# Kernel optimization log

Hardware: AMD Instinct MI355X
Metric: run time of the kernel (lower is better)

The kernel has to match this reference:

```python
import jax, jax.numpy as jnp
import numpy as np

B, S, D, F, E, K = 4, 2048, 512, 1024, 8, 2

def setup_inputs() -> dict:
    key = jax.random.key(0)
    ks = jax.random.split(key, 7)
    hidden = jax.random.normal(ks[0], (B, S, D), dtype=jnp.float32)
    top_k_indices = jax.random.randint(ks[1], (B, S, K), 0, E, dtype=jnp.int32)
    top_k_weights = jax.random.uniform(ks[2], (B, S, K), dtype=jnp.float32)
    scale1 = 1.0 / np.sqrt(D)
    scale2 = 1.0 / np.sqrt(F)
    W1 = jax.random.normal(ks[3], (E, D, F), dtype=jnp.float32) * scale1
    b1 = jnp.zeros((E, F), dtype=jnp.float32)
    W2 = jax.random.normal(ks[4], (E, F, D), dtype=jnp.float32) * scale2
    b2 = jnp.zeros((E, D), dtype=jnp.float32)
    return {"hidden": hidden, "top_k_indices": top_k_indices,
            "top_k_weights": top_k_weights, "W1": W1, "b1": b1, "W2": W2, "b2": b2}

def reference(hidden, top_k_indices, top_k_weights, W1, b1, W2, b2):
    b, s, d = hidden.shape
    e = W1.shape[0]
    x = hidden.reshape(-1, d)                      # [T, D]
    idx = top_k_indices.reshape(-1, top_k_indices.shape[-1])   # [T, K]
    w = top_k_weights.reshape(-1, top_k_weights.shape[-1])     # [T, K]
    # combine weight per (token, expert): sum over k slots routed to expert e
    onehot = jax.nn.one_hot(idx, e, dtype=w.dtype)             # [T, K, E]
    cw = jnp.einsum('tk,tke->et', w, onehot)                   # [E, T]
    def step(acc, params):
        W1e, b1e, W2e, b2e, cwe = params
        h = jax.nn.gelu(x @ W1e + b1e)                         # [T, F]
        y = h @ W2e + b2e                                      # [T, D]
        return acc + cwe[:, None] * y, None
    out, _ = jax.lax.scan(step, jnp.zeros_like(x), (W1, b1, W2, b2, cw))
    return out.reshape(b, s, d)
```

## Files before the change

kernel.cpp:

```cpp
#include <hip/hip_runtime.h>
#include <hip/hip_bf16.h>

#define T_TOK 8192
#define DDIM  512
#define FDIM  1024
#define NEXP  8
#define KTOP  2
#define NSLOT (T_TOK * KTOP)
#define MAX_ROWS 17408
#define MAX_T128 136

#define NB_CAST 512
#define NB_T    4096
#define PREP_BLOCKS (1 + NB_CAST + NB_T + NB_T)

typedef __attribute__((ext_vector_type(8))) __bf16 bf16x8;
typedef __attribute__((ext_vector_type(4))) __bf16 bf16x4;
typedef __attribute__((ext_vector_type(4))) float  f32x4;
typedef __attribute__((ext_vector_type(8))) unsigned short u16x8;

typedef __attribute__((address_space(1))) const unsigned int* gp1;
typedef __attribute__((address_space(3))) unsigned int*       lp3;
#define GL2LDS(g, l) __builtin_amdgcn_global_load_lds((gp1)(const void*)(g), (lp3)(void*)(l), 16, 0, 0)


__device__ __forceinline__ float gelu_fast(float x){
    float u = 0.7978845608028654f * (x + 0.044715f * x * x * x);
    return x / (1.0f + __expf(-2.0f * u));
}

__device__ __forceinline__ unsigned short f2bf(float v){
    __hip_bfloat16 b = __float2bfloat16(v);
    return *(unsigned short*)&b;
}

__global__ __launch_bounds__(1024) void prep_kernel(
    const float* __restrict__ x, const int* __restrict__ idx,
    const float* __restrict__ W1, const float* __restrict__ W2,
    unsigned short* __restrict__ xbf,
    unsigned short* __restrict__ w1t, unsigned short* __restrict__ w2t,
    int* __restrict__ meta, int2* __restrict__ map,
    int* __restrict__ list, int* __restrict__ slot2row)
{
    __shared__ unsigned long long sA[1024], sB[1024];
    __shared__ unsigned short tile[32][33];
    const int b   = blockIdx.x;
    const int tid = threadIdx.x;

    if (b == 0){
        const int base = tid * 16;
        int mye[16];
        unsigned long long a = 0, bb = 0;
        #pragma unroll
        for (int i = 0; i < 16; i++){
            int e = idx[base + i] & 7;
            mye[i] = e;
            unsigned long long one = 1ull << (16 * (e & 3));
            if (e < 4) a += one; else bb += one;
        }
        sA[tid] = a; sB[tid] = bb;
        __syncthreads();
        for (int off = 1; off < 1024; off <<= 1){
            unsigned long long ta = 0, tb = 0;
            if (tid >= off){ ta = sA[tid - off]; tb = sB[tid - off]; }
            __syncthreads();
            sA[tid] += ta; sB[tid] += tb;
            __syncthreads();
        }
        const unsigned long long iA = sA[tid],  iB = sB[tid];
        const unsigned long long tA = sA[1023], tB = sB[1023];

        int cnt[NEXP], pad[NEXP], off_e[NEXP], tc[NEXP + 1];
        tc[0] = 0;
        int o = 0;
        #pragma unroll
        for (int e = 0; e < NEXP; e++){
            unsigned long long src = (e < 4) ? tA : tB;
            cnt[e] = (int)((src >> (16 * (e & 3))) & 0xffffull);
            pad[e] = (cnt[e] + 127) & ~127;
            off_e[e] = o; o += pad[e];
            tc[e + 1] = tc[e] + (pad[e] >> 7);
        }
        const int nrows = o, nt = tc[NEXP];

        if (tid == 0) meta[16] = nt;
        if (tid < NEXP) meta[17 + tid] = off_e[tid];
        if (tid < nt){
            int e = 0;
            while (tid >= tc[e + 1]) e++;
            map[tid] = make_int2(e, off_e[e] + (tid - tc[e]) * 128);
        }

        int run[NEXP];
        #pragma unroll
        for (int e = 0; e < NEXP; e++){
            unsigned long long isrc = (e < 4) ? iA : iB;
            unsigned long long csrc = (e < 4) ? a  : bb;
            int incl = (int)((isrc >> (16 * (e & 3))) & 0xffffull);
            int ce   = (int)((csrc >> (16 * (e & 3))) & 0xffffull);
            run[e] = off_e[e] + incl - ce;
        }
        #pragma unroll
        for (int i = 0; i < 16; i++){
            int e = mye[i];
            int gg = run[e]++;
            list[gg] = (base + i) >> 1;
            slot2row[base + i] = gg;
        }
        for (int p = tid; p < nrows; p += 1024){
            #pragma unroll
            for (int e = 0; e < NEXP; e++){
                if (p >= off_e[e] + cnt[e] && p < off_e[e] + pad[e]) list[p] = 0;
            }
        }
    } else if (b < 1 + NB_CAST){
        int i = (b - 1) * 1024 + tid;
        const float4* s = (const float4*)x;
        float4 va = s[2 * i];
        float4 vb = s[2 * i + 1];
        u16x8 ov;
        ov[0] = f2bf(va.x); ov[1] = f2bf(va.y); ov[2] = f2bf(va.z); ov[3] = f2bf(va.w);
        ov[4] = f2bf(vb.x); ov[5] = f2bf(vb.y); ov[6] = f2bf(vb.z); ov[7] = f2bf(vb.w);
        *(u16x8*)(xbf + (size_t)i * 8) = ov;
    } else {
        int blk = b - (1 + NB_CAST);
        const float* src; unsigned short* dst; int R, C, cpb_shift, cpb_mask;
        if (blk < NB_T){ src = W1; dst = w1t; R = DDIM; C = FDIM; cpb_shift = 5; cpb_mask = 31; }
        else           { src = W2; dst = w2t; R = FDIM; C = DDIM; cpb_shift = 4; cpb_mask = 15; blk -= NB_T; }
        int e   = blk >> 9;
        int rem = blk & 511;
        int rb  = rem >> cpb_shift, cb = rem & cpb_mask;
        int r0 = rb * 32, c0 = cb * 32;
        int tx = tid & 31, ty = tid >> 5;
        const float* sf = src + (size_t)e * R * C;
        unsigned short* d = dst + (size_t)e * R * C;
        tile[ty][tx] = f2bf(sf[(size_t)(r0 + ty) * C + c0 + tx]);
        __syncthreads();
        d[(size_t)(c0 + ty) * R + r0 + tx] = tile[tx][ty];
    }
}

__global__ __launch_bounds__(256, 2) void gemm1_kernel(
    const unsigned short* __restrict__ x,
    const unsigned short* __restrict__ w1t,
    const float* __restrict__ b1,
    const int* __restrict__ meta,
    const int2* __restrict__ map,
    const int* __restrict__ list,
    unsigned short* __restrict__ h)
{
    const int ntiles = meta[16];
    const int nwg = ntiles * (FDIM / 128);
    int id = blockIdx.y * gridDim.x + blockIdx.x;
    if (id >= nwg) return;
    int q = nwg >> 3, r = nwg & 7;
    int xcd = id & 7, rank = id >> 3;
    int swz = (xcd < r) ? (xcd * (q + 1) + rank)
                        : (r * (q + 1) + (xcd - r) * q + rank);
    const int tile = swz >> 3;
    const int n0 = (swz & 7) * 128;
    int2 em = map[tile];
    const int e = em.x, grow0 = em.y;

    __shared__ __align__(16) unsigned short smem[16384];
    unsigned short* As = smem;
    unsigned short* Bs = smem + 8192;

    const int tid  = threadIdx.x;
    const int wave = tid >> 6;
    const int lane = tid & 63;
    const int rl   = lane >> 2;
    const int kq   = lane & 3;

    const int row0 = wave * 16 + rl;
    const int row1 = 64 + wave * 16 + rl;

    const unsigned short* pA0 = x + (size_t)list[grow0 + row0] * DDIM + kq * 8;
    const unsigned short* pA1 = x + (size_t)list[grow0 + row1] * DDIM + kq * 8;
    const unsigned short* pB0 = w1t + ((size_t)e * FDIM + n0 + row0) * DDIM + kq * 8;
    const unsigned short* pB1 = w1t + ((size_t)e * FDIM + n0 + row1) * DDIM + kq * 8;

    char* lA = (char*)As + wave * 1024;
    char* lB = (char*)Bs + wave * 1024;

    const int quad = lane >> 4, lrow = lane & 15;
    const int wr = (wave >> 1) * 64;
    const int wc = (wave & 1) * 64;

    f32x4 acc[4][4];
    #pragma unroll
    for (int i = 0; i < 4; i++)
        #pragma unroll
        for (int j = 0; j < 4; j++) acc[i][j] = (f32x4)0.0f;

    for (int kk = 0; kk < DDIM; kk += 64){
        __syncthreads();
        GL2LDS(pA0 + kk,      lA);
        GL2LDS(pA1 + kk,      lA + 4096);
        GL2LDS(pA0 + kk + 32, lA + 8192);
        GL2LDS(pA1 + kk + 32, lA + 12288);
        GL2LDS(pB0 + kk,      lB);
        GL2LDS(pB1 + kk,      lB + 4096);
        GL2LDS(pB0 + kk + 32, lB + 8192);
        GL2LDS(pB1 + kk + 32, lB + 12288);
        __syncthreads();
        bf16x8 a[4][2], b[4][2];
        #pragma unroll
        for (int i = 0; i < 4; i++){
            #pragma unroll
            for (int ks = 0; ks < 2; ks++){
                a[i][ks] = *(const bf16x8*)&As[ks * 4096 + (wr + i * 16 + lrow) * 32 + quad * 8];
                b[i][ks] = *(const bf16x8*)&Bs[ks * 4096 + (wc + i * 16 + lrow) * 32 + quad * 8];
            }
        }
        #pragma unroll
        for (int i = 0; i < 4; i++){
            #pragma unroll
            for (int j = 0; j < 4; j++){
                acc[i][j] = __builtin_amdgcn_mfma_f32_16x16x32_bf16(a[i][0], b[j][0], acc[i][j], 0, 0, 0);
                acc[i][j] = __builtin_amdgcn_mfma_f32_16x16x32_bf16(a[i][1], b[j][1], acc[i][j], 0, 0, 0);
            }
        }
    }

    __syncthreads();
    #pragma unroll
    for (int j = 0; j < 4; j++){
        int C = wc + j * 16 + lrow;
        float bias = b1[e * FDIM + n0 + C];
        #pragma unroll
        for (int i = 0; i < 4; i++){
            #pragma unroll
            for (int rr = 0; rr < 4; rr++){
                int R = wr + i * 16 + quad * 4 + rr;
                smem[R * 128 + (C ^ (((R >> 2) & 7) << 4))] =
                    f2bf(gelu_fast(acc[i][j][rr] + bias));
            }
        }
    }
    __syncthreads();
    #pragma unroll
    for (int p = 0; p < 8; p++){
        int idx = p * 2048 + tid * 8;
        int R = idx >> 7, C = idx & 127;
        u16x8 v = *(const u16x8*)&smem[R * 128 + (C ^ (((R >> 2) & 7) << 4))];
        *(u16x8*)&h[(size_t)(grow0 + R) * FDIM + n0 + C] = v;
    }
}

__global__ __launch_bounds__(256, 2) void gemm2_kernel(
    const unsigned short* __restrict__ h,
    const unsigned short* __restrict__ w2t,
    const float* __restrict__ b2,
    const int* __restrict__ meta,
    const int2* __restrict__ map,
    unsigned short* __restrict__ y)
{
    const int ntiles = meta[16];
    const int nwg = ntiles * (DDIM / 128);
    int id = blockIdx.y * gridDim.x + blockIdx.x;
    if (id >= nwg) return;
    int q = nwg >> 3, r = nwg & 7;
    int xcd = id & 7, rank = id >> 3;
    int swz = (xcd < r) ? (xcd * (q + 1) + rank)
                        : (r * (q + 1) + (xcd - r) * q + rank);
    const int tile = swz >> 2;
    const int n0 = (swz & 3) * 128;
    int2 em = map[tile];
    const int e = em.x, grow0 = em.y;

    __shared__ __align__(16) unsigned short smem[16384];
    unsigned short* As = smem;
    unsigned short* Bs = smem + 8192;

    const int tid  = threadIdx.x;
    const int wave = tid >> 6;
    const int lane = tid & 63;
    const int rl   = lane >> 2;
    const int kq   = lane & 3;

    const int row0 = wave * 16 + rl;
    const int row1 = 64 + wave * 16 + rl;

    const unsigned short* pA0 = h + (size_t)(grow0 + row0) * FDIM + kq * 8;
    const unsigned short* pA1 = h + (size_t)(grow0 + row1) * FDIM + kq * 8;
    const unsigned short* pB0 = w2t + ((size_t)e * DDIM + n0 + row0) * FDIM + kq * 8;
    const unsigned short* pB1 = w2t + ((size_t)e * DDIM + n0 + row1) * FDIM + kq * 8;

    char* lA = (char*)As + wave * 1024;
    char* lB = (char*)Bs + wave * 1024;

    const int quad = lane >> 4, lrow = lane & 15;
    const int wr = (wave >> 1) * 64;
    const int wc = (wave & 1) * 64;

    f32x4 acc[4][4];
    #pragma unroll
    for (int i = 0; i < 4; i++)
        #pragma unroll
        for (int j = 0; j < 4; j++) acc[i][j] = (f32x4)0.0f;

    for (int kk = 0; kk < FDIM; kk += 64){
        __syncthreads();
        GL2LDS(pA0 + kk,      lA);
        GL2LDS(pA1 + kk,      lA + 4096);
        GL2LDS(pA0 + kk + 32, lA + 8192);
        GL2LDS(pA1 + kk + 32, lA + 12288);
        GL2LDS(pB0 + kk,      lB);
        GL2LDS(pB1 + kk,      lB + 4096);
        GL2LDS(pB0 + kk + 32, lB + 8192);
        GL2LDS(pB1 + kk + 32, lB + 12288);
        __syncthreads();
        bf16x8 a[4][2], b[4][2];
        #pragma unroll
        for (int i = 0; i < 4; i++){
            #pragma unroll
            for (int ks = 0; ks < 2; ks++){
                a[i][ks] = *(const bf16x8*)&As[ks * 4096 + (wr + i * 16 + lrow) * 32 + quad * 8];
                b[i][ks] = *(const bf16x8*)&Bs[ks * 4096 + (wc + i * 16 + lrow) * 32 + quad * 8];
            }
        }
        #pragma unroll
        for (int i = 0; i < 4; i++){
            #pragma unroll
            for (int j = 0; j < 4; j++){
                acc[i][j] = __builtin_amdgcn_mfma_f32_16x16x32_bf16(a[i][0], b[j][0], acc[i][j], 0, 0, 0);
                acc[i][j] = __builtin_amdgcn_mfma_f32_16x16x32_bf16(a[i][1], b[j][1], acc[i][j], 0, 0, 0);
            }
        }
    }

    __syncthreads();
    #pragma unroll
    for (int j = 0; j < 4; j++){
        int C = wc + j * 16 + lrow;
        float bias = b2[e * DDIM + n0 + C];
        #pragma unroll
        for (int i = 0; i < 4; i++){
            #pragma unroll
            for (int rr = 0; rr < 4; rr++){
                int R = wr + i * 16 + quad * 4 + rr;
                smem[R * 128 + (C ^ (((R >> 2) & 7) << 4))] =
                    f2bf(acc[i][j][rr] + bias);
            }
        }
    }
    __syncthreads();
    #pragma unroll
    for (int p = 0; p < 8; p++){
        int idx = p * 2048 + tid * 8;
        int R = idx >> 7, C = idx & 127;
        u16x8 v = *(const u16x8*)&smem[R * 128 + (C ^ (((R >> 2) & 7) << 4))];
        *(u16x8*)&y[(size_t)(grow0 + R) * DDIM + n0 + C] = v;
    }
}

__global__ void combine_kernel(const unsigned short* __restrict__ y,
                               const int* __restrict__ slot2row,
                               const float* __restrict__ wk,
                               float* __restrict__ out){
    int g = blockIdx.x * blockDim.x + threadIdx.x;
    int t = g >> 7, seg = g & 127;
    int ra = slot2row[2 * t], rb = slot2row[2 * t + 1];
    float wa = wk[2 * t];
    float wb = wk[2 * t + 1];
    bf16x4 ya = *(const bf16x4*)(y + (size_t)ra * DDIM + seg * 4);
    bf16x4 yb = *(const bf16x4*)(y + (size_t)rb * DDIM + seg * 4);
    float4 o;
    o.x = wa * (float)ya[0] + wb * (float)yb[0];
    o.y = wa * (float)ya[1] + wb * (float)yb[1];
    o.z = wa * (float)ya[2] + wb * (float)yb[2];
    o.w = wa * (float)ya[3] + wb * (float)yb[3];
    *(float4*)(out + (size_t)t * DDIM + seg * 4) = o;
}

extern "C" void kernel_launch(void* const* d_in, const int* in_sizes, int n_in,
                              void* d_out, int out_size, void* d_ws, size_t ws_size,
                              hipStream_t stream){
    const float* x   = (const float*)d_in[0];
    const int*   idx = (const int*)d_in[1];
    const float* wk  = (const float*)d_in[2];
    const float* W1  = (const float*)d_in[3];
    const float* b1  = (const float*)d_in[4];
    const float* W2  = (const float*)d_in[5];
    const float* b2  = (const float*)d_in[6];
    float* out = (float*)d_out;

    char* ws = (char*)d_ws;
    int*   meta     = (int*)ws;
    int2*  map      = (int2*)(ws + 512);
    int*   list     = (int*)(ws + 4096);
    int*   slot2row = (int*)(ws + 81920);
    unsigned short* xbf = (unsigned short*)(ws + 262144);
    unsigned short* w1t = (unsigned short*)(ws + 8650752);
    unsigned short* w2t = (unsigned short*)(ws + 17039360);
    unsigned short* h   = (unsigned short*)(ws + 25427968);
    unsigned short* y   = (unsigned short*)(ws + 61079552);
    if (ws_size < 78905344u) return;

    prep_kernel<<<PREP_BLOCKS, 1024, 0, stream>>>(
        x, idx, W1, W2, xbf, w1t, w2t, meta, map, list, slot2row);

    gemm1_kernel<<<dim3(FDIM / 128, MAX_T128), 256, 0, stream>>>(
        xbf, w1t, b1, meta, map, list, h);

    gemm2_kernel<<<dim3(DDIM / 128, MAX_T128), 256, 0, stream>>>(
        h, w2t, b2, meta, map, y);

    combine_kernel<<<(T_TOK * DDIM / 4) / 256, 256, 0, stream>>>(y, slot2row, wk, out);
}
```

Baseline: 178.1 us.

## Widen gemm1 tile to 128x256 with per-wave full-row, 64-column layout

Expands the first expert GEMM's output tile from 128x128 to 128x256, so each workgroup covers 256 F-columns and half as many workgroups are launched. Each wave now computes all 128 rows by 64 columns (8x4 MFMA accumulators), raising arithmetic intensity per loaded A fragment and halving redundant gathers of token rows. In exchange it uses more LDS (48KB) and doubles accumulator registers, which may reduce occupancy. The epilogue is split into two 64-row halves to fit the staging buffer.

```diff
diff --git a/kernel.cpp b/kernel.cpp
--- a/kernel.cpp
+++ b/kernel.cpp
@@ -150,19 +150,19 @@
     unsigned short* __restrict__ h)
 {
     const int ntiles = meta[16];
-    const int nwg = ntiles * (FDIM / 128);
+    const int nwg = ntiles * (FDIM / 256);
     int id = blockIdx.y * gridDim.x + blockIdx.x;
     if (id >= nwg) return;
     int q = nwg >> 3, r = nwg & 7;
     int xcd = id & 7, rank = id >> 3;
     int swz = (xcd < r) ? (xcd * (q + 1) + rank)
                         : (r * (q + 1) + (xcd - r) * q + rank);
-    const int tile = swz >> 3;
-    const int n0 = (swz & 7) * 128;
+    const int tile = swz >> 2;
+    const int n0 = (swz & 3) * 256;
     int2 em = map[tile];
     const int e = em.x, grow0 = em.y;
 
-    __shared__ __align__(16) unsigned short smem[16384];
+    __shared__ __align__(16) unsigned short smem[24576];
     unsigned short* As = smem;
     unsigned short* Bs = smem + 8192;
 
@@ -172,24 +172,25 @@
     const int rl   = lane >> 2;
     const int kq   = lane & 3;
 
-    const int row0 = wave * 16 + rl;
-    const int row1 = 64 + wave * 16 + rl;
-
-    const unsigned short* pA0 = x + (size_t)list[grow0 + row0] * DDIM + kq * 8;
-    const unsigned short* pA1 = x + (size_t)list[grow0 + row1] * DDIM + kq * 8;
-    const unsigned short* pB0 = w1t + ((size_t)e * FDIM + n0 + row0) * DDIM + kq * 8;
-    const unsigned short* pB1 = w1t + ((size_t)e * FDIM + n0 + row1) * DDIM + kq * 8;
+    const int rA0 = wave * 16 + rl;
+    const int rA1 = 64 + wave * 16 + rl;
+
+    const unsigned short* pA0 = x + (size_t)list[grow0 + rA0] * DDIM + kq * 8;
+    const unsigned short* pA1 = x + (size_t)list[grow0 + rA1] * DDIM + kq * 8;
+    const unsigned short* pB0 = w1t + ((size_t)e * FDIM + n0 +   0 + wave * 16 + rl) * DDIM + kq * 8;
+    const unsigned short* pB1 = w1t + ((size_t)e * FDIM + n0 +  64 + wave * 16 + rl) * DDIM + kq * 8;
+    const unsigned short* pB2 = w1t + ((size_t)e * FDIM + n0 + 128 + wave * 16 + rl) * DDIM + kq * 8;
+    const unsigned short* pB3 = w1t + ((size_t)e * FDIM + n0 + 192 + wave * 16 + rl) * DDIM + kq * 8;
 
     char* lA = (char*)As + wave * 1024;
     char* lB = (char*)Bs + wave * 1024;
 
     const int quad = lane >> 4, lrow = lane & 15;
-    const int wr = (wave >> 1) * 64;
-    const int wc = (wave & 1) * 64;
-
-    f32x4 acc[4][4];
+    const int wc = wave * 64;
+
+    f32x4 acc[8][4];
     #pragma unroll
-    for (int i = 0; i < 4; i++)
+    for (int i = 0; i < 8; i++)
         #pragma unroll
         for (int j = 0; j < 4; j++) acc[i][j] = (f32x4)0.0f;
 
@@ -201,50 +202,55 @@
         GL2LDS(pA1 + kk + 32, lA + 12288);
         GL2LDS(pB0 + kk,      lB);
         GL2LDS(pB1 + kk,      lB + 4096);
-        GL2LDS(pB0 + kk + 32, lB + 8192);
-        GL2LDS(pB1 + kk + 32, lB + 12288);
-        __syncthreads();
-        bf16x8 a[4][2], b[4][2];
-        #pragma unroll
-        for (int i = 0; i < 4; i++){
-            #pragma unroll
-            for (int ks = 0; ks < 2; ks++){
-                a[i][ks] = *(const bf16x8*)&As[ks * 4096 + (wr + i * 16 + lrow) * 32 + quad * 8];
-                b[i][ks] = *(const bf16x8*)&Bs[ks * 4096 + (wc + i * 16 + lrow) * 32 + quad * 8];
+        GL2LDS(pB2 + kk,      lB + 8192);
+        GL2LDS(pB3 + kk,      lB + 12288);
+        GL2LDS(pB0 + kk + 32, lB + 16384);
+        GL2LDS(pB1 + kk + 32, lB + 20480);
+        GL2LDS(pB2 + kk + 32, lB + 24576);
+        GL2LDS(pB3 + kk + 32, lB + 28672);
+        __syncthreads();
+        #pragma unroll
+        for (int ks = 0; ks < 2; ks++){
+            bf16x8 a[8], b[4];
+            #pragma unroll
+            for (int i = 0; i < 8; i++)
+                a[i] = *(const bf16x8*)&As[ks * 4096 + (i * 16 + lrow) * 32 + quad * 8];
+            #pragma unroll
+            for (int j = 0; j < 4; j++)
+                b[j] = *(const bf16x8*)&Bs[ks * 8192 + (wc + j * 16 + lrow) * 32 + quad * 8];
+            #pragma unroll
+            for (int i = 0; i < 8; i++)
+                #pragma unroll
+                for (int j = 0; j < 4; j++)
+                    acc[i][j] = __builtin_amdgcn_mfma_f32_16x16x32_bf16(a[i], b[j], acc[i][j], 0, 0, 0);
+        }
+    }
+
+    #pragma unroll
+    for (int half = 0; half < 2; half++){
+        __syncthreads();
+        #pragma unroll
+        for (int j = 0; j < 4; j++){
+            int C = wc + j * 16 + lrow;
+            float bias = b1[e * FDIM + n0 + C];
+            #pragma unroll
+            for (int ii = 0; ii < 4; ii++){
+                #pragma unroll
+                for (int rr = 0; rr < 4; rr++){
+                    int R = ii * 16 + quad * 4 + rr;
+                    smem[R * 256 + (C ^ (((R >> 2) & 7) << 4))] =
+                        f2bf(gelu_fast(acc[half * 4 + ii][j][rr] + bias));
+                }
             }
         }
-        #pragma unroll
-        for (int i = 0; i < 4; i++){
-            #pragma unroll
-            for (int j = 0; j < 4; j++){
-                acc[i][j] = __builtin_amdgcn_mfma_f32_16x16x32_bf16(a[i][0], b[j][0], acc[i][j], 0, 0, 0);
-                acc[i][j] = __builtin_amdgcn_mfma_f32_16x16x32_bf16(a[i][1], b[j][1], acc[i][j], 0, 0, 0);
-            }
-        }
-    }
-
-    __syncthreads();
-    #pragma unroll
-    for (int j = 0; j < 4; j++){
-        int C = wc + j * 16 + lrow;
-        float bias = b1[e * FDIM + n0 + C];
-        #pragma unroll
-        for (int i = 0; i < 4; i++){
-            #pragma unroll
-            for (int rr = 0; rr < 4; rr++){
-                int R = wr + i * 16 + quad * 4 + rr;
-                smem[R * 128 + (C ^ (((R >> 2) & 7) << 4))] =
-                    f2bf(gelu_fast(acc[i][j][rr] + bias));
-            }
-        }
-    }
-    __syncthreads();
-    #pragma unroll
-    for (int p = 0; p < 8; p++){
-        int idx = p * 2048 + tid * 8;
-        int R = idx >> 7, C = idx & 127;
-        u16x8 v = *(const u16x8*)&smem[R * 128 + (C ^ (((R >> 2) & 7) << 4))];
-        *(u16x8*)&h[(size_t)(grow0 + R) * FDIM + n0 + C] = v;
+        __syncthreads();
+        #pragma unroll
+        for (int p = 0; p < 8; p++){
+            int idx2 = p * 2048 + tid * 8;
+            int R = idx2 >> 8, C = idx2 & 255;
+            u16x8 v = *(const u16x8*)&smem[R * 256 + (C ^ (((R >> 2) & 7) << 4))];
+            *(u16x8*)&h[(size_t)(grow0 + half * 64 + R) * FDIM + n0 + C] = v;
+        }
     }
 }
 
@@ -401,7 +407,7 @@
     prep_kernel<<<PREP_BLOCKS, 1024, 0, stream>>>(
         x, idx, W1, W2, xbf, w1t, w2t, meta, map, list, slot2row);
 
-    gemm1_kernel<<<dim3(FDIM / 128, MAX_T128), 256, 0, stream>>>(
+    gemm1_kernel<<<dim3(FDIM / 256, MAX_T128), 256, 0, stream>>>(
         xbf, w1t, b1, meta, map, list, h);
 
     gemm2_kernel<<<dim3(DDIM / 128, MAX_T128), 256, 0, stream>>>(
```

Measured after the change: 192.5 us. +8.1%, slower.
